# Performance work log

Measured on AMD Instinct MI355X. Metric: run time of the kernel, lower is better.

## Reference

```python
import jax, jax.numpy as jnp
import numpy as np

B, S, D, E, H = 4, 2048, 1024, 8, 4096  # batch, seq, d_model, n_experts, ffn hidden (4*d_model)


def setup_inputs() -> dict:
    key = jax.random.key(0)
    ks = jax.random.split(key, 4)
    s = 0.02  # init scale
    return {
        "x": jax.random.normal(ks[0], (B, S, D), dtype=jnp.float32),
        "router_w": jax.random.normal(ks[1], (E, D), dtype=jnp.float32) * s,
        "router_b": jnp.zeros((E,), dtype=jnp.float32),
        "w1": jax.random.normal(ks[2], (E, D, H), dtype=jnp.float32) * s,
        "b1": jnp.zeros((E, H), dtype=jnp.float32),
        "w2": jax.random.normal(ks[3], (E, H, D), dtype=jnp.float32) * s,
        "b2": jnp.zeros((E, D), dtype=jnp.float32),
        "top_k": 2,
    }


def reference(x, router_w, router_b, w1, b1, w2, b2, top_k):
    # Router logits [B, S, E]
    logits = jnp.einsum('bsd,ed->bse', x, router_w) + router_b
    # Top-k selection; scatter top-k logits into a -inf tensor, then softmax
    # => gate weight is exactly 0 for non-selected experts.
    top_v, top_i = jax.lax.top_k(logits, top_k)           # [B, S, k]
    sel = jax.nn.one_hot(top_i, logits.shape[-1], dtype=bool).any(axis=-2)  # [B, S, E]
    gate = jax.nn.softmax(jnp.where(sel, logits, -jnp.inf), axis=-1)        # [B, S, E]

    # Dense sum over experts (mathematically identical to the masked
    # gather/scatter loop since non-selected gates are exactly 0).
    out = jnp.zeros_like(x)
    for e in range(w1.shape[0]):  # small fixed expert loop keeps peak memory low
        h = jax.nn.relu(x @ w1[e] + b1[e])        # [B, S, H]
        out = out + (h @ w2[e] + b2[e]) * gate[..., e:e + 1]
    return out
```

## Files before the change

### kernel.cpp

```cpp
#include <hip/hip_runtime.h>
#include <hip/hip_bf16.h>

#define NTOK   8192
#define DMODEL 1024
#define NEXP   8
#define HFFN   4096
#define NSLOT  16384
#define MAXWL  136

typedef __bf16 bf16x8 __attribute__((ext_vector_type(8)));
typedef float  f32x4  __attribute__((ext_vector_type(4)));
typedef unsigned short u16;
typedef u16 u16x8 __attribute__((ext_vector_type(8)));

typedef const __attribute__((address_space(1))) void* gas_ptr;
typedef __attribute__((address_space(3))) void* las_ptr;

__device__ inline u16 f2b(float f) {
  __hip_bfloat16 h = __float2bfloat16(f);
  return *reinterpret_cast<u16*>(&h);
}
__device__ inline float b2f(u16 u) {
  unsigned int v = ((unsigned int)u) << 16;
  return *reinterpret_cast<float*>(&v);
}

__global__ void router_k(const float* __restrict__ x, const float* __restrict__ rw,
                         const float* __restrict__ rb, int* __restrict__ tok_e,
                         float* __restrict__ tok_g, int* __restrict__ counts) {
  __shared__ int h[NEXP];
  int tid = threadIdx.x;
  if (tid < NEXP) h[tid] = 0;
  __syncthreads();
  int wave = tid >> 6, lane = tid & 63;
  int t = blockIdx.x * 4 + wave;
  const float* xr = x + (size_t)t * DMODEL;
  float acc[NEXP];
#pragma unroll
  for (int e = 0; e < NEXP; e++) acc[e] = 0.f;
#pragma unroll
  for (int i = 0; i < 4; i++) {
    int d = i * 256 + lane * 4;
    float4 xv = *(const float4*)(xr + d);
#pragma unroll
    for (int e = 0; e < NEXP; e++) {
      float4 wv = *(const float4*)(rw + (size_t)e * DMODEL + d);
      acc[e] += xv.x * wv.x + xv.y * wv.y + xv.z * wv.z + xv.w * wv.w;
    }
  }
#pragma unroll
  for (int e = 0; e < NEXP; e++) {
#pragma unroll
    for (int off = 32; off > 0; off >>= 1) acc[e] += __shfl_xor(acc[e], off);
  }
  if (lane == 0) {
    float lg[NEXP];
#pragma unroll
    for (int e = 0; e < NEXP; e++) lg[e] = acc[e] + rb[e];
    int e0 = 0;
#pragma unroll
    for (int e = 1; e < NEXP; e++) if (lg[e] > lg[e0]) e0 = e;
    int e1 = (e0 == 0) ? 1 : 0;
#pragma unroll
    for (int e = 0; e < NEXP; e++) if (e != e0 && lg[e] > lg[e1]) e1 = e;
    float ex = expf(lg[e1] - lg[e0]);
    float g0 = 1.f / (1.f + ex);
    float g1 = ex / (1.f + ex);
    tok_e[2 * t]     = e0;  tok_e[2 * t + 1] = e1;
    tok_g[2 * t]     = g0;  tok_g[2 * t + 1] = g1;
    atomicAdd(&h[e0], 1);
    atomicAdd(&h[e1], 1);
  }
  __syncthreads();
  if (tid < NEXP && h[tid]) atomicAdd(&counts[tid], h[tid]);
}

__global__ void offsets_k(const int* __restrict__ counts, int* __restrict__ offsets,
                          int* __restrict__ wl) {
  if (threadIdx.x == 0) {
    int s = 0;
    for (int e = 0; e < NEXP; e++) { offsets[e] = s; s += counts[e]; }
    offsets[NEXP] = s;
    int n = 0;
    for (int e = 0; e < NEXP; e++)
      for (int t = 0; t * 128 < counts[e]; ++t) wl[n++] = (e << 16) | t;
    for (int i = n; i < MAXWL; ++i) wl[i] = -1;
  }
}

__global__ void assign_k(const int* __restrict__ tok_e, int* __restrict__ cursors,
                         const int* __restrict__ offsets, int* __restrict__ row_tok,
                         int* __restrict__ slot_of) {
  __shared__ int h[NEXP], base[NEXP];
  int tid = threadIdx.x;
  if (tid < NEXP) h[tid] = 0;
  __syncthreads();
  int t = blockIdx.x * 256 + tid;
  int e0 = tok_e[2 * t], e1 = tok_e[2 * t + 1];
  int r0 = atomicAdd(&h[e0], 1);
  int r1 = atomicAdd(&h[e1], 1);
  __syncthreads();
  if (tid < NEXP) base[tid] = atomicAdd(&cursors[tid], h[tid]);
  __syncthreads();
  int s0 = offsets[e0] + base[e0] + r0;
  int s1 = offsets[e1] + base[e1] + r1;
  row_tok[s0] = t;  slot_of[2 * t] = s0;
  row_tok[s1] = t;  slot_of[2 * t + 1] = s1;
}

__global__ void gather_k(const float* __restrict__ x, const int* __restrict__ row_tok,
                         u16* __restrict__ xbg) {
  int idx = blockIdx.x * 256 + threadIdx.x;
  int s = idx >> 8;
  int c = (idx & 255) * 4;
  int t = row_tok[s];
  float4 v = *(const float4*)(x + (size_t)t * DMODEL + c);
  ushort4 o;
  o.x = f2b(v.x); o.y = f2b(v.y); o.z = f2b(v.z); o.w = f2b(v.w);
  *(ushort4*)(xbg + (size_t)s * DMODEL + c) = o;
}

__global__ void wtrans_k(const float* __restrict__ src, u16* __restrict__ dst,
                         int R, int C) {
  __shared__ u16 tile[64][72];
  int e = blockIdx.z;
  int r0 = blockIdx.x * 64, c0 = blockIdx.y * 64;
  int tid = threadIdx.x;
  int tr = tid >> 2, tc = (tid & 3) * 16;
  const float* sp = src + (size_t)e * R * C + (size_t)(r0 + tr) * C + c0 + tc;
#pragma unroll
  for (int i = 0; i < 16; i += 4) {
    float4 v = *(const float4*)(sp + i);
    tile[tr][tc + i]     = f2b(v.x);
    tile[tr][tc + i + 1] = f2b(v.y);
    tile[tr][tc + i + 2] = f2b(v.z);
    tile[tr][tc + i + 3] = f2b(v.w);
  }
  __syncthreads();
  u16* dbase = dst + (size_t)e * R * C;
#pragma unroll
  for (int it = 0; it < 2; ++it) {
    int oc  = it * 32 + (tid >> 3);
    int seg = (tid & 7) * 8;
    u16x8 o;
#pragma unroll
    for (int j = 0; j < 8; ++j) o[j] = tile[seg + j][oc];
    *(u16x8*)(dbase + (size_t)(c0 + oc) * R + r0 + seg) = o;
  }
}

template <int KTOT, int KCHUNK, int NTOT, int NY, bool RELU, bool BIAS>
__global__ __launch_bounds__(256, 4) void moe_gemm_k(
    const u16* __restrict__ A, const u16* __restrict__ Bt,
    const float* __restrict__ bias, u16* __restrict__ Out,
    const int* __restrict__ counts, const int* __restrict__ offsets,
    const int* __restrict__ wl) {
  __shared__ __align__(16) u16 Als[2 * 128 * 32];
  __shared__ __align__(16) u16 Bls[2 * 128 * 32];

  int nwg = gridDim.x;
  int lid = blockIdx.x;
  int orig = (lid & 7) * (nwg >> 3) + (lid >> 3);
  int kq   = orig / (MAXWL * NY);
  int r1   = orig - kq * (MAXWL * NY);
  int xp   = r1 / (NY * 2);
  int r2   = r1 - xp * (NY * 2);
  int xt = (xp << 1) | (r2 & 1);
  int y  = r2 >> 1;
  int w = wl[xt];
  if (w < 0) return;
  int e   = w >> 16;
  int tr0 = (w & 0xffff) << 7;
  int cnt = counts[e];
  int seg = offsets[e];
  int n0  = y << 7;

  int tid = threadIdx.x;
  int wid = tid >> 6, lane = tid & 63;
  int wm = wid >> 1, wn = wid & 1;
  int l15 = lane & 15, lhi = lane >> 4;

  int co = (((tid & 3) ^ ((tid >> 3) & 3)) << 3) + kq * KCHUNK;
  const u16* gA0 = A + (size_t)(seg + tr0 + (tid >> 2)) * KTOT + co;
  const u16* gA1 = gA0 + (size_t)64 * KTOT;
  const u16* Bte = Bt + (size_t)e * NTOT * KTOT;
  const u16* gB0 = Bte + (size_t)(n0 + (tid >> 2)) * KTOT + co;
  const u16* gB1 = gB0 + (size_t)64 * KTOT;
  char* Ab = (char*)Als;
  char* Bb = (char*)Bls;
  int sdst = wid << 10;

  auto stage = [&](int bs, int kb) {
    __builtin_amdgcn_global_load_lds((gas_ptr)(gA0 + kb), (las_ptr)(Ab + bs * 8192 + sdst), 16, 0, 0);
    __builtin_amdgcn_global_load_lds((gas_ptr)(gA1 + kb), (las_ptr)(Ab + bs * 8192 + 4096 + sdst), 16, 0, 0);
    __builtin_amdgcn_global_load_lds((gas_ptr)(gB0 + kb), (las_ptr)(Bb + bs * 8192 + sdst), 16, 0, 0);
    __builtin_amdgcn_global_load_lds((gas_ptr)(gB1 + kb), (las_ptr)(Bb + bs * 8192 + 4096 + sdst), 16, 0, 0);
  };

  int xsw = ((lhi ^ ((l15 >> 1) & 3)) << 4);
  int aoff = (wm * 64 + l15) * 64 + xsw;
  int boff = (wn * 64 + l15) * 64 + xsw;

  f32x4 acc[4][4] = {};
  constexpr int NT = KCHUNK / 32;

  stage(0, 0);
  for (int kt = 0; kt < NT; ++kt) {
    int cur = kt & 1;
    if (kt + 1 < NT) {
      stage(cur ^ 1, (kt + 1) * 32);
      asm volatile("s_waitcnt vmcnt(4)" ::: "memory");
    } else {
      asm volatile("s_waitcnt vmcnt(0)" ::: "memory");
    }
    __builtin_amdgcn_s_barrier();
    __builtin_amdgcn_sched_barrier(0);

    const char* ab = Ab + cur * 8192;
    const char* bb = Bb + cur * 8192;
    bf16x8 af[4], bv[4];
#pragma unroll
    for (int m = 0; m < 4; ++m) af[m] = *(const bf16x8*)(ab + aoff + m * 1024);
#pragma unroll
    for (int n = 0; n < 4; ++n) bv[n] = *(const bf16x8*)(bb + boff + n * 1024);
#pragma unroll
    for (int m = 0; m < 4; ++m)
#pragma unroll
      for (int n = 0; n < 4; ++n)
        acc[m][n] = __builtin_amdgcn_mfma_f32_16x16x32_bf16(af[m], bv[n], acc[m][n], 0, 0, 0);
    __builtin_amdgcn_s_barrier();
  }

  u16* outp = Out + (size_t)kq * ((size_t)NSLOT * NTOT);

  int cb = n0 + wn * 64 + l15;
  float bs4[4] = {0.f, 0.f, 0.f, 0.f};
  if (BIAS) {
    const float* bias_e = bias + (size_t)e * NTOT;
#pragma unroll
    for (int n = 0; n < 4; ++n) bs4[n] = bias_e[cb + n * 16];
  }
  int rb0 = tr0 + wm * 64 + lhi * 4;
#pragma unroll
  for (int m = 0; m < 4; ++m) {
#pragma unroll
    for (int r = 0; r < 4; ++r) {
      int gi = rb0 + m * 16 + r;
      if (gi >= cnt) continue;
      size_t orow = (size_t)(seg + gi) * NTOT + cb;
#pragma unroll
      for (int n = 0; n < 4; ++n) {
        float v = acc[m][n][r] + bs4[n];
        if (RELU) v = fmaxf(v, 0.f);
        outp[orow + n * 16] = f2b(v);
      }
    }
  }
}

__global__ void combine_k(const u16* __restrict__ Y, const int* __restrict__ slot_of,
                          const int* __restrict__ tok_e, const float* __restrict__ tok_g,
                          const float* __restrict__ b2, float* __restrict__ out) {
  int t = blockIdx.x;
  int d = threadIdx.x * 4;
  int s0 = slot_of[2 * t], s1 = slot_of[2 * t + 1];
  int e0 = tok_e[2 * t],  e1 = tok_e[2 * t + 1];
  float g0 = tok_g[2 * t], g1 = tok_g[2 * t + 1];
  const u16* Y1 = Y + (size_t)NSLOT * DMODEL;
  ushort4 a0 = *(const ushort4*)(Y  + (size_t)s0 * DMODEL + d);
  ushort4 a1 = *(const ushort4*)(Y1 + (size_t)s0 * DMODEL + d);
  ushort4 c0 = *(const ushort4*)(Y  + (size_t)s1 * DMODEL + d);
  ushort4 c1 = *(const ushort4*)(Y1 + (size_t)s1 * DMODEL + d);
  float4 b20 = *(const float4*)(b2 + (size_t)e0 * DMODEL + d);
  float4 b21 = *(const float4*)(b2 + (size_t)e1 * DMODEL + d);
  float4 o;
  o.x = g0 * (b2f(a0.x) + b2f(a1.x) + b20.x) + g1 * (b2f(c0.x) + b2f(c1.x) + b21.x);
  o.y = g0 * (b2f(a0.y) + b2f(a1.y) + b20.y) + g1 * (b2f(c0.y) + b2f(c1.y) + b21.y);
  o.z = g0 * (b2f(a0.z) + b2f(a1.z) + b20.z) + g1 * (b2f(c0.z) + b2f(c1.z) + b21.z);
  o.w = g0 * (b2f(a0.w) + b2f(a1.w) + b20.w) + g1 * (b2f(c0.w) + b2f(c1.w) + b21.w);
  *(float4*)(out + (size_t)t * DMODEL + d) = o;
}

extern "C" void kernel_launch(void* const* d_in, const int* in_sizes, int n_in,
                              void* d_out, int out_size, void* d_ws, size_t ws_size,
                              hipStream_t stream) {
  const float* x  = (const float*)d_in[0];
  const float* rw = (const float*)d_in[1];
  const float* rb = (const float*)d_in[2];
  const float* w1 = (const float*)d_in[3];
  const float* b1 = (const float*)d_in[4];
  const float* w2 = (const float*)d_in[5];
  const float* b2 = (const float*)d_in[6];

  char* ws = (char*)d_ws;
  size_t o = 0;
  u16* w1t = (u16*)(ws + o); o += (size_t)NEXP * HFFN * DMODEL * 2;
  u16* w2t = (u16*)(ws + o); o += (size_t)NEXP * HFFN * DMODEL * 2;
  u16* xbg = (u16*)(ws + o); o += (size_t)(NSLOT + 256) * DMODEL * 2;
  u16* hc  = (u16*)(ws + o); o += (size_t)(NSLOT + 256) * HFFN * 2;
  u16* yp  = (u16*)w1t;
  int*   tok_e   = (int*)(ws + o);   o += NTOK * 2 * sizeof(int);
  float* tok_g   = (float*)(ws + o); o += NTOK * 2 * sizeof(float);
  int*   slot_of = (int*)(ws + o);   o += NTOK * 2 * sizeof(int);
  int*   row_tok = (int*)(ws + o);   o += NSLOT * sizeof(int);
  int*   meta    = (int*)(ws + o);   o += 32 * sizeof(int);
  int*   wl      = (int*)(ws + o);   o += MAXWL * sizeof(int);
  int* counts  = meta;
  int* cursors = meta + 8;
  int* offsets = meta + 16;

  hipMemsetAsync(meta, 0, 64, stream);
  router_k<<<NTOK / 4, 256, 0, stream>>>(x, rw, rb, tok_e, tok_g, counts);
  offsets_k<<<1, 64, 0, stream>>>(counts, offsets, wl);
  assign_k<<<NTOK / 256, 256, 0, stream>>>(tok_e, cursors, offsets, row_tok, slot_of);
  gather_k<<<NSLOT, 256, 0, stream>>>(x, row_tok, xbg);
  wtrans_k<<<dim3(DMODEL / 64, HFFN / 64, NEXP), 256, 0, stream>>>(w1, w1t, DMODEL, HFFN);
  wtrans_k<<<dim3(HFFN / 64, DMODEL / 64, NEXP), 256, 0, stream>>>(w2, w2t, HFFN, DMODEL);

  moe_gemm_k<DMODEL, DMODEL, HFFN, HFFN / 128, true, true>
      <<<MAXWL * (HFFN / 128), 256, 0, stream>>>(
          xbg, w1t, b1, hc, counts, offsets, wl);
  moe_gemm_k<HFFN, HFFN / 2, DMODEL, DMODEL / 128, false, false>
      <<<MAXWL * (DMODEL / 128) * 2, 256, 0, stream>>>(
          hc, w2t, nullptr, yp, counts, offsets, wl);

  combine_k<<<NTOK, 256, 0, stream>>>(yp, slot_of, tok_e, tok_g, b2, (float*)d_out);
}
```

Before: 516.1 us.

## Fuse gather into first GEMM and combine into second GEMM via atomics

The router now writes a bf16 copy of x, and the first expert GEMM gathers token rows through a row_tok index table in shared memory, which removes the separate gather kernel. The second GEMM adds bias, applies the gate weight and accumulates into the fp32 output with atomicAdd. This removes the bf16 partial-output buffers and the combine kernel. The cost is a full memset of the output and many scattered float atomics (two k-splits times two experts per element), and the summation order is no longer deterministic.

```diff
diff --git a/kernel.cpp b/kernel.cpp
--- a/kernel.cpp
+++ b/kernel.cpp
@@ -20,14 +20,11 @@
   __hip_bfloat16 h = __float2bfloat16(f);
   return *reinterpret_cast<u16*>(&h);
 }
-__device__ inline float b2f(u16 u) {
-  unsigned int v = ((unsigned int)u) << 16;
-  return *reinterpret_cast<float*>(&v);
-}
 
 __global__ void router_k(const float* __restrict__ x, const float* __restrict__ rw,
                          const float* __restrict__ rb, int* __restrict__ tok_e,
-                         float* __restrict__ tok_g, int* __restrict__ counts) {
+                         float* __restrict__ tok_g, int* __restrict__ counts,
+                         u16* __restrict__ xb) {
   __shared__ int h[NEXP];
   int tid = threadIdx.x;
   if (tid < NEXP) h[tid] = 0;
@@ -42,6 +39,9 @@
   for (int i = 0; i < 4; i++) {
     int d = i * 256 + lane * 4;
     float4 xv = *(const float4*)(xr + d);
+    ushort4 o;
+    o.x = f2b(xv.x); o.y = f2b(xv.y); o.z = f2b(xv.z); o.w = f2b(xv.w);
+    *(ushort4*)(xb + (size_t)t * DMODEL + d) = o;
 #pragma unroll
     for (int e = 0; e < NEXP; e++) {
       float4 wv = *(const float4*)(rw + (size_t)e * DMODEL + d);
@@ -88,9 +88,9 @@
   }
 }
 
-__global__ void assign_k(const int* __restrict__ tok_e, int* __restrict__ cursors,
-                         const int* __restrict__ offsets, int* __restrict__ row_tok,
-                         int* __restrict__ slot_of) {
+__global__ void assign_k(const int* __restrict__ tok_e, const float* __restrict__ tok_g,
+                         int* __restrict__ cursors, const int* __restrict__ offsets,
+                         int* __restrict__ row_tok, float* __restrict__ slot_g) {
   __shared__ int h[NEXP], base[NEXP];
   int tid = threadIdx.x;
   if (tid < NEXP) h[tid] = 0;
@@ -104,20 +104,8 @@
   __syncthreads();
   int s0 = offsets[e0] + base[e0] + r0;
   int s1 = offsets[e1] + base[e1] + r1;
-  row_tok[s0] = t;  slot_of[2 * t] = s0;
-  row_tok[s1] = t;  slot_of[2 * t + 1] = s1;
-}
-
-__global__ void gather_k(const float* __restrict__ x, const int* __restrict__ row_tok,
-                         u16* __restrict__ xbg) {
-  int idx = blockIdx.x * 256 + threadIdx.x;
-  int s = idx >> 8;
-  int c = (idx & 255) * 4;
-  int t = row_tok[s];
-  float4 v = *(const float4*)(x + (size_t)t * DMODEL + c);
-  ushort4 o;
-  o.x = f2b(v.x); o.y = f2b(v.y); o.z = f2b(v.z); o.w = f2b(v.w);
-  *(ushort4*)(xbg + (size_t)s * DMODEL + c) = o;
+  row_tok[s0] = t;  slot_g[s0] = tok_g[2 * t];
+  row_tok[s1] = t;  slot_g[s1] = tok_g[2 * t + 1];
 }
 
 __global__ void wtrans_k(const float* __restrict__ src, u16* __restrict__ dst,
@@ -149,14 +137,16 @@
   }
 }
 
-template <int KTOT, int KCHUNK, int NTOT, int NY, bool RELU, bool BIAS>
+template <int KTOT, int KCHUNK, int NTOT, int NY, bool RELU, bool GATHER, bool ATOMIC>
 __global__ __launch_bounds__(256, 4) void moe_gemm_k(
     const u16* __restrict__ A, const u16* __restrict__ Bt,
-    const float* __restrict__ bias, u16* __restrict__ Out,
+    const float* __restrict__ bias, u16* __restrict__ Out, float* __restrict__ fout,
     const int* __restrict__ counts, const int* __restrict__ offsets,
-    const int* __restrict__ wl) {
+    const int* __restrict__ wl, const int* __restrict__ row_tok,
+    const float* __restrict__ slot_g) {
   __shared__ __align__(16) u16 Als[2 * 128 * 32];
   __shared__ __align__(16) u16 Bls[2 * 128 * 32];
+  __shared__ int srow[128];
 
   int nwg = gridDim.x;
   int lid = blockIdx.x;
@@ -176,13 +166,23 @@
   int n0  = y << 7;
 
   int tid = threadIdx.x;
+  if (GATHER) {
+    if (tid < 128) {
+      int idx = tr0 + tid;
+      if (idx > cnt - 1) idx = cnt - 1;
+      srow[tid] = row_tok[seg + idx];
+    }
+    __syncthreads();
+  }
+
   int wid = tid >> 6, lane = tid & 63;
   int wm = wid >> 1, wn = wid & 1;
   int l15 = lane & 15, lhi = lane >> 4;
 
   int co = (((tid & 3) ^ ((tid >> 3) & 3)) << 3) + kq * KCHUNK;
-  const u16* gA0 = A + (size_t)(seg + tr0 + (tid >> 2)) * KTOT + co;
-  const u16* gA1 = gA0 + (size_t)64 * KTOT;
+  int ar0 = tid >> 2, ar1 = 64 + (tid >> 2);
+  const u16* gA0 = A + (size_t)(GATHER ? srow[ar0] : (seg + tr0 + ar0)) * KTOT + co;
+  const u16* gA1 = A + (size_t)(GATHER ? srow[ar1] : (seg + tr0 + ar1)) * KTOT + co;
   const u16* Bte = Bt + (size_t)e * NTOT * KTOT;
   const u16* gB0 = Bte + (size_t)(n0 + (tid >> 2)) * KTOT + co;
   const u16* gB1 = gB0 + (size_t)64 * KTOT;
@@ -231,54 +231,48 @@
     __builtin_amdgcn_s_barrier();
   }
 
-  u16* outp = Out + (size_t)kq * ((size_t)NSLOT * NTOT);
-
   int cb = n0 + wn * 64 + l15;
-  float bs4[4] = {0.f, 0.f, 0.f, 0.f};
-  if (BIAS) {
+  int rb0 = tr0 + wm * 64 + lhi * 4;
+  if (ATOMIC) {
+    const float* b2e = bias + (size_t)e * NTOT;
+    float bs4[4];
+#pragma unroll
+    for (int n = 0; n < 4; ++n) bs4[n] = (kq == 0) ? b2e[cb + n * 16] : 0.f;
+#pragma unroll
+    for (int m = 0; m < 4; ++m) {
+#pragma unroll
+      for (int r = 0; r < 4; ++r) {
+        int gi = rb0 + m * 16 + r;
+        if (gi >= cnt) continue;
+        int tok = row_tok[seg + gi];
+        float g = slot_g[seg + gi];
+        float* orow = fout + (size_t)tok * NTOT + cb;
+#pragma unroll
+        for (int n = 0; n < 4; ++n)
+          atomicAdd(&orow[n * 16], (acc[m][n][r] + bs4[n]) * g);
+      }
+    }
+  } else {
     const float* bias_e = bias + (size_t)e * NTOT;
+    float bs4[4];
 #pragma unroll
     for (int n = 0; n < 4; ++n) bs4[n] = bias_e[cb + n * 16];
-  }
-  int rb0 = tr0 + wm * 64 + lhi * 4;
-#pragma unroll
-  for (int m = 0; m < 4; ++m) {
-#pragma unroll
-    for (int r = 0; r < 4; ++r) {
-      int gi = rb0 + m * 16 + r;
-      if (gi >= cnt) continue;
-      size_t orow = (size_t)(seg + gi) * NTOT + cb;
-#pragma unroll
-      for (int n = 0; n < 4; ++n) {
-        float v = acc[m][n][r] + bs4[n];
-        if (RELU) v = fmaxf(v, 0.f);
-        outp[orow + n * 16] = f2b(v);
+#pragma unroll
+    for (int m = 0; m < 4; ++m) {
+#pragma unroll
+      for (int r = 0; r < 4; ++r) {
+        int gi = rb0 + m * 16 + r;
+        if (gi >= cnt) continue;
+        size_t orow = (size_t)(seg + gi) * NTOT + cb;
+#pragma unroll
+        for (int n = 0; n < 4; ++n) {
+          float v = acc[m][n][r] + bs4[n];
+          if (RELU) v = fmaxf(v, 0.f);
+          Out[orow + n * 16] = f2b(v);
+        }
       }
     }
   }
-}
-
-__global__ void combine_k(const u16* __restrict__ Y, const int* __restrict__ slot_of,
-                          const int* __restrict__ tok_e, const float* __restrict__ tok_g,
-                          const float* __restrict__ b2, float* __restrict__ out) {
-  int t = blockIdx.x;
-  int d = threadIdx.x * 4;
-  int s0 = slot_of[2 * t], s1 = slot_of[2 * t + 1];
-  int e0 = tok_e[2 * t],  e1 = tok_e[2 * t + 1];
-  float g0 = tok_g[2 * t], g1 = tok_g[2 * t + 1];
-  const u16* Y1 = Y + (size_t)NSLOT * DMODEL;
-  ushort4 a0 = *(const ushort4*)(Y  + (size_t)s0 * DMODEL + d);
-  ushort4 a1 = *(const ushort4*)(Y1 + (size_t)s0 * DMODEL + d);
-  ushort4 c0 = *(const ushort4*)(Y  + (size_t)s1 * DMODEL + d);
-  ushort4 c1 = *(const ushort4*)(Y1 + (size_t)s1 * DMODEL + d);
-  float4 b20 = *(const float4*)(b2 + (size_t)e0 * DMODEL + d);
-  float4 b21 = *(const float4*)(b2 + (size_t)e1 * DMODEL + d);
-  float4 o;
-  o.x = g0 * (b2f(a0.x) + b2f(a1.x) + b20.x) + g1 * (b2f(c0.x) + b2f(c1.x) + b21.x);
-  o.y = g0 * (b2f(a0.y) + b2f(a1.y) + b20.y) + g1 * (b2f(c0.y) + b2f(c1.y) + b21.y);
-  o.z = g0 * (b2f(a0.z) + b2f(a1.z) + b20.z) + g1 * (b2f(c0.z) + b2f(c1.z) + b21.z);
-  o.w = g0 * (b2f(a0.w) + b2f(a1.w) + b20.w) + g1 * (b2f(c0.w) + b2f(c1.w) + b21.w);
-  *(float4*)(out + (size_t)t * DMODEL + d) = o;
 }
 
 extern "C" void kernel_launch(void* const* d_in, const int* in_sizes, int n_in,
@@ -296,13 +290,12 @@
   size_t o = 0;
   u16* w1t = (u16*)(ws + o); o += (size_t)NEXP * HFFN * DMODEL * 2;
   u16* w2t = (u16*)(ws + o); o += (size_t)NEXP * HFFN * DMODEL * 2;
-  u16* xbg = (u16*)(ws + o); o += (size_t)(NSLOT + 256) * DMODEL * 2;
+  u16* xb  = (u16*)(ws + o); o += (size_t)NTOK * DMODEL * 2;
   u16* hc  = (u16*)(ws + o); o += (size_t)(NSLOT + 256) * HFFN * 2;
-  u16* yp  = (u16*)w1t;
   int*   tok_e   = (int*)(ws + o);   o += NTOK * 2 * sizeof(int);
   float* tok_g   = (float*)(ws + o); o += NTOK * 2 * sizeof(float);
-  int*   slot_of = (int*)(ws + o);   o += NTOK * 2 * sizeof(int);
   int*   row_tok = (int*)(ws + o);   o += NSLOT * sizeof(int);
+  float* slot_g  = (float*)(ws + o); o += NSLOT * sizeof(float);
   int*   meta    = (int*)(ws + o);   o += 32 * sizeof(int);
   int*   wl      = (int*)(ws + o);   o += MAXWL * sizeof(int);
   int* counts  = meta;
@@ -310,19 +303,17 @@
   int* offsets = meta + 16;
 
   hipMemsetAsync(meta, 0, 64, stream);
-  router_k<<<NTOK / 4, 256, 0, stream>>>(x, rw, rb, tok_e, tok_g, counts);
+  hipMemsetAsync(d_out, 0, (size_t)NTOK * DMODEL * sizeof(float), stream);
+  router_k<<<NTOK / 4, 256, 0, stream>>>(x, rw, rb, tok_e, tok_g, counts, xb);
   offsets_k<<<1, 64, 0, stream>>>(counts, offsets, wl);
-  assign_k<<<NTOK / 256, 256, 0, stream>>>(tok_e, cursors, offsets, row_tok, slot_of);
-  gather_k<<<NSLOT, 256, 0, stream>>>(x, row_tok, xbg);
+  assign_k<<<NTOK / 256, 256, 0, stream>>>(tok_e, tok_g, cursors, offsets, row_tok, slot_g);
   wtrans_k<<<dim3(DMODEL / 64, HFFN / 64, NEXP), 256, 0, stream>>>(w1, w1t, DMODEL, HFFN);
   wtrans_k<<<dim3(HFFN / 64, DMODEL / 64, NEXP), 256, 0, stream>>>(w2, w2t, HFFN, DMODEL);
 
-  moe_gemm_k<DMODEL, DMODEL, HFFN, HFFN / 128, true, true>
+  moe_gemm_k<DMODEL, DMODEL, HFFN, HFFN / 128, true, true, false>
       <<<MAXWL * (HFFN / 128), 256, 0, stream>>>(
-          xbg, w1t, b1, hc, counts, offsets, wl);
-  moe_gemm_k<HFFN, HFFN / 2, DMODEL, DMODEL / 128, false, false>
+          xb, w1t, b1, hc, nullptr, counts, offsets, wl, row_tok, slot_g);
+  moe_gemm_k<HFFN, HFFN / 2, DMODEL, DMODEL / 128, false, false, true>
       <<<MAXWL * (DMODEL / 128) * 2, 256, 0, stream>>>(
-          hc, w2t, nullptr, yp, counts, offsets, wl);
-
-  combine_k<<<NTOK, 256, 0, stream>>>(yp, slot_of, tok_e, tok_g, b2, (float*)d_out);
-}
+          hc, w2t, b2, nullptr, (float*)d_out, counts, offsets, wl, row_tok, slot_g);
+}
```

Result: slower. 547.1 us (+6.0%).
